# Optimization experiments

Measured on AMD Instinct MI355X. Metric: run time of the kernel, lower is better.

The kernel has to match this reference:

```python
import jax, jax.numpy as jnp
import numpy as np

N_COMP = 36          # sdf_n_comp
GRID = 300           # gridSize per axis
SDF_DIM = 256
APP_DIM = 128
MULTIRES = 3         # sdf positional-encoding octaves -> 3 + 3*2*3 = 21 channels
N_PTS = 524288       # sample points per batch (~1024 rays x 512 samples)
EMB_CH = 3 + 3 * 2 * MULTIRES            # 21
IN_CH = EMB_CH + 3 * N_COMP              # 129
OUT_CH = 1 + APP_DIM                     # 129 (sdf + appearance feature)
INIT_RADIUS = 0.2


def setup_inputs() -> dict:
    key = jax.random.key(0)
    ks = jax.random.split(key, 6)
    xyz_sampled = jax.random.uniform(ks[0], (N_PTS, 3), jnp.float32) * 2.0 - 1.0
    # tensor-decomposition grids (stacked over the 3 VM planes)
    planes = jax.random.normal(ks[1], (3, N_COMP, GRID, GRID), jnp.float32) * 0.1
    lines = jax.random.normal(ks[2], (3, N_COMP, GRID), jnp.float32) * (1.0 / (N_COMP * 3))
    # sdf_mat MLP params, initialized per init_mlp()
    w1 = jax.random.normal(ks[3], (SDF_DIM, IN_CH), jnp.float32) * (np.sqrt(2.0) / np.sqrt(SDF_DIM))
    b1 = jnp.zeros((SDF_DIM,), jnp.float32)
    w2 = jax.random.normal(ks[4], (OUT_CH, SDF_DIM), jnp.float32) * 1e-4 + np.sqrt(np.pi) / np.sqrt(SDF_DIM)
    b2 = jnp.full((OUT_CH,), -INIT_RADIUS, jnp.float32)
    return {"xyz_sampled": xyz_sampled, "planes": planes, "lines": lines,
            "w1": w1, "b1": b1, "w2": w2, "b2": b2}


def _bilin2d(plane, x, y):
    """Bilinear grid_sample, align_corners=True. plane [C,H,W]; x,y [N] in [-1,1] -> [C,N]."""
    C, H, W = plane.shape
    fx = (x + 1.0) * 0.5 * (W - 1)
    fy = (y + 1.0) * 0.5 * (H - 1)
    x0 = jnp.clip(jnp.floor(fx).astype(jnp.int32), 0, W - 2)
    y0 = jnp.clip(jnp.floor(fy).astype(jnp.int32), 0, H - 2)
    tx = fx - x0
    ty = fy - y0
    v00 = plane[:, y0, x0]
    v01 = plane[:, y0, x0 + 1]
    v10 = plane[:, y0 + 1, x0]
    v11 = plane[:, y0 + 1, x0 + 1]
    return (v00 * (1 - tx) * (1 - ty) + v01 * tx * (1 - ty)
            + v10 * (1 - tx) * ty + v11 * tx * ty)


def _lin1d(line, z):
    """Linear grid_sample, align_corners=True. line [C,L]; z [N] in [-1,1] -> [C,N]."""
    C, L = line.shape
    fz = (z + 1.0) * 0.5 * (L - 1)
    z0 = jnp.clip(jnp.floor(fz).astype(jnp.int32), 0, L - 2)
    tz = fz - z0
    return line[:, z0] * (1 - tz) + line[:, z0 + 1] * tz


def _embed(x):
    """NeRF positional encoding, include_input, octaves 2^0..2^(MULTIRES-1). [N,3] -> [N,21]."""
    freqs = 2.0 ** jnp.arange(MULTIRES, dtype=x.dtype)
    ang = x[:, :, None] * freqs  # [N,3,MULTIRES]
    n = x.shape[0]
    return jnp.concatenate([x, jnp.sin(ang).reshape(n, -1), jnp.cos(ang).reshape(n, -1)], axis=-1)


def reference(xyz_sampled, planes, lines, w1, b1, w2, b2):
    # aabb = [-1,1]^3 -> normalization is identity, kept explicit for faithfulness
    xn = (xyz_sampled - (-1.0)) / 2.0 * 2.0 - 1.0
    # matMode=[[0,1],[0,2],[1,2]], vecMode=[2,1,0]
    px = jnp.stack([xn[:, 0], xn[:, 0], xn[:, 1]])  # [3,N] first plane coord
    py = jnp.stack([xn[:, 1], xn[:, 2], xn[:, 2]])  # [3,N] second plane coord
    pz = jnp.stack([xn[:, 2], xn[:, 1], xn[:, 0]])  # [3,N] line coord
    pf = jax.vmap(_bilin2d)(planes, px, py)         # [3,C,N]
    lf = jax.vmap(_lin1d)(lines, pz)                # [3,C,N]
    feat = (pf * lf).transpose(2, 0, 1).reshape(xn.shape[0], -1)  # [N, 3*C]
    mlp_in = jnp.concatenate([_embed(xyz_sampled), feat], axis=-1)  # [N, 129]
    h = jax.nn.softplus(100.0 * (mlp_in @ w1.T + b1)) / 100.0       # Softplus(beta=100)
    out = h @ w2.T + b2                                             # [N, 1+app_dim]
    return out
```

## Files before the change

kernel.cpp:

```cpp
#include <hip/hip_runtime.h>
#include <hip/hip_bf16.h>
#include <cstdint>
#include <cstddef>


using half2v = __attribute__((ext_vector_type(2))) _Float16;
using half4  = __attribute__((ext_vector_type(4))) _Float16;
using half8  = __attribute__((ext_vector_type(8))) _Float16;
using floatx4 = __attribute__((ext_vector_type(4))) float;

#define NPTS    524288
#define GRES    300
#define NCOMP   36
#define SDFD    256
#define IN_CH   129
#define IN_PAD  160
#define OUT_CH  129
#define OUT_PAD 144
#define TILE_M  64
#define S_IN    168
#define S_H     264

#define OFF_W1S 0
#define SZ_W1S  (5*4*256*8*2)
#define OFF_W2S (OFF_W1S + SZ_W1S)
#define SZ_W2S  (8*4*144*8*2)
#define OFF_PLT (OFF_W2S + SZ_W2S)
#define SZ_PLT  (3*300*300*36*2)
#define OFF_LT  (OFF_PLT + SZ_PLT)
#define SZ_LT   (3*300*36*2)
#define WS_NEED_FAST ((size_t)(OFF_LT + SZ_LT))


__global__ void prep_planes_k(const float* __restrict__ planes, _Float16* __restrict__ pl_t) {
    int idx = blockIdx.x * 256 + threadIdx.x;
    if (idx >= 3 * GRES * GRES) return;
    int x = idx % GRES; int t = idx / GRES; int y = t % GRES; int m = t / GRES;
    _Float16* dst = pl_t + (size_t)idx * NCOMP;
    const float* src = planes + (size_t)m * NCOMP * GRES * GRES + (size_t)y * GRES + x;
    #pragma unroll
    for (int c4 = 0; c4 < NCOMP; c4 += 4) {
        half4 o;
        #pragma unroll
        for (int i = 0; i < 4; ++i)
            o[i] = (_Float16)src[(size_t)(c4 + i) * GRES * GRES];
        *(half4*)(dst + c4) = o;
    }
}

#define NB_W1 ((5*4*256*8 + 255)/256)
#define NB_W2 ((8*4*144*8 + 255)/256)
#define NB_L  ((3*GRES + 255)/256)
__global__ void prep_small_k(const float* __restrict__ w1, const float* __restrict__ w2,
                             const float* __restrict__ lines,
                             _Float16* __restrict__ w1s, _Float16* __restrict__ w2s,
                             _Float16* __restrict__ l_t) {
    int b = blockIdx.x;
    if (b < NB_W1) {
        int t = b * 256 + threadIdx.x;
        if (t >= 5 * 4 * 256 * 8) return;
        int j = t & 7; int n = (t >> 3) & 255; int q = t >> 11;
        int k = (q >> 2) * 32 + (q & 3) * 8 + j;
        float v = 0.f;
        if (k < IN_CH) {
            int ko = (k < 108) ? (21 + k) : (k - 108);
            v = w1[n * IN_CH + ko];
        }
        w1s[t] = (_Float16)v;
    } else if (b < NB_W1 + NB_W2) {
        int t = (b - NB_W1) * 256 + threadIdx.x;
        if (t >= 8 * 4 * 144 * 8) return;
        int j = t & 7; int r = t >> 3; int n = r % 144; int q = r / 144;
        int k = (q >> 2) * 32 + (q & 3) * 8 + j;
        float v = (n < OUT_CH) ? w2[n * SDFD + k] : 0.f;
        w2s[t] = (_Float16)v;
    } else {
        int idx = (b - NB_W1 - NB_W2) * 256 + threadIdx.x;
        if (idx >= 3 * GRES) return;
        int z = idx % GRES; int m = idx / GRES;
        _Float16* dst = l_t + (size_t)idx * NCOMP;
        const float* src = lines + ((size_t)m * NCOMP) * GRES + z;
        for (int c = 0; c < NCOMP; ++c)
            dst[c] = (_Float16)src[(size_t)c * GRES];
    }
}


__device__ __forceinline__ float softplus100(float z) {
    return fmaxf(z, 0.f) + __logf(1.f + __expf(-fabsf(z)));
}

template <bool FAST>
__global__ __launch_bounds__(256, 2)
void tsdf_fused_k(const float* __restrict__ xyz,
                  const float* __restrict__ planes,
                  const float* __restrict__ lines,
                  const _Float16* __restrict__ pl_t,
                  const _Float16* __restrict__ l_t,
                  const _Float16* __restrict__ w1s,
                  const _Float16* __restrict__ w2s,
                  const float* __restrict__ b1,
                  const float* __restrict__ b2,
                  float* __restrict__ out)
{
    __shared__ _Float16 mlp_lds[TILE_M * S_IN];
    __shared__ _Float16 h_lds[TILE_M * S_H];
    const int tid = threadIdx.x;
    const int blk = blockIdx.x;

    {
        const int p   = tid >> 2;
        const int sub = tid & 3;
        const size_t gp = (size_t)blk * TILE_M + p;
        const float X = xyz[gp * 3 + 0];
        const float Y = xyz[gp * 3 + 1];
        const float Z = xyz[gp * 3 + 2];
        if (sub < 3) {
            const int m = sub;
            const float px = (m == 2) ? Y : X;
            const float py = (m == 0) ? Y : Z;
            const float pz = (m == 0) ? Z : ((m == 1) ? Y : X);
            float fx = (px + 1.f) * 0.5f * 299.f;
            float fy = (py + 1.f) * 0.5f * 299.f;
            float fz = (pz + 1.f) * 0.5f * 299.f;
            int x0 = (int)floorf(fx); x0 = x0 < 0 ? 0 : (x0 > 298 ? 298 : x0);
            int y0 = (int)floorf(fy); y0 = y0 < 0 ? 0 : (y0 > 298 ? 298 : y0);
            int z0 = (int)floorf(fz); z0 = z0 < 0 ? 0 : (z0 > 298 ? 298 : z0);
            const float tx = fx - (float)x0, ty = fy - (float)y0, tz = fz - (float)z0;
            const float w00 = (1.f - tx) * (1.f - ty), w01 = tx * (1.f - ty);
            const float w10 = (1.f - tx) * ty,         w11 = tx * ty;
            const float lw0 = 1.f - tz, lw1 = tz;
            _Float16* dst = &mlp_lds[p * S_IN + m * NCOMP];
            if (FAST) {
                const _Float16 h00 = (_Float16)w00, h01 = (_Float16)w01;
                const _Float16 h10 = (_Float16)w10, h11 = (_Float16)w11;
                const _Float16 hl0 = (_Float16)lw0, hl1 = (_Float16)lw1;
                const half4 W00 = {h00, h00, h00, h00}, W01 = {h01, h01, h01, h01};
                const half4 W10 = {h10, h10, h10, h10}, W11 = {h11, h11, h11, h11};
                const half4 WL0 = {hl0, hl0, hl0, hl0}, WL1 = {hl1, hl1, hl1, hl1};
                const _Float16* b00 = pl_t + ((size_t)(m * GRES + y0) * GRES + x0) * NCOMP;
                const _Float16* lb  = l_t + (size_t)(m * GRES + z0) * NCOMP;
                #pragma unroll
                for (int c = 0; c < NCOMP; c += 4) {
                    half4 v00 = *(const half4*)(b00 + c);
                    half4 v01 = *(const half4*)(b00 + NCOMP + c);
                    half4 v10 = *(const half4*)(b00 + GRES * NCOMP + c);
                    half4 v11 = *(const half4*)(b00 + GRES * NCOMP + NCOMP + c);
                    half4 l0  = *(const half4*)(lb + c);
                    half4 l1  = *(const half4*)(lb + NCOMP + c);
                    half4 pf = v00 * W00 + v01 * W01 + v10 * W10 + v11 * W11;
                    half4 lf = l0 * WL0 + l1 * WL1;
                    *(half4*)(dst + c) = pf * lf;
                }
            } else {
                const float* pb = planes + (size_t)m * NCOMP * GRES * GRES;
                for (int c = 0; c < NCOMP; ++c) {
                    const float* pc = pb + (size_t)c * GRES * GRES + (size_t)y0 * GRES + x0;
                    const float* lc = lines + ((size_t)m * NCOMP + c) * GRES + z0;
                    float pf = pc[0] * w00 + pc[1] * w01 + pc[GRES] * w10 + pc[GRES + 1] * w11;
                    float lf = lc[0] * lw0 + lc[1] * lw1;
                    dst[c] = (_Float16)(pf * lf);
                }
            }
        } else {
            _Float16* e = &mlp_lds[p * S_IN];
            e[108] = (_Float16)X; e[109] = (_Float16)Y; e[110] = (_Float16)Z;
            const float v3[3] = {X, Y, Z};
            #pragma unroll
            for (int d = 0; d < 3; ++d) {
                float f = 1.f;
                #pragma unroll
                for (int q = 0; q < 3; ++q) {
                    const float a = v3[d] * f;
                    e[111 + d * 3 + q] = (_Float16)__sinf(a);
                    e[120 + d * 3 + q] = (_Float16)__cosf(a);
                    f *= 2.f;
                }
            }
            e[129] = (_Float16)0.f;
            #pragma unroll
            for (int k = 130; k < IN_PAD; k += 2)
                *(half2v*)&e[k] = (half2v){(_Float16)0.f, (_Float16)0.f};
        }
    }
    __syncthreads();

    const int lane = tid & 63;
    const int wv   = tid >> 6;
    const int l15  = lane & 15;
    const int quad = lane >> 4;

    floatx4 acc1[4][4];
    #pragma unroll
    for (int mt = 0; mt < 4; ++mt)
        #pragma unroll
        for (int nt = 0; nt < 4; ++nt)
            acc1[mt][nt] = (floatx4){0.f, 0.f, 0.f, 0.f};

    #pragma unroll
    for (int s = 0; s < 5; ++s) {
        half8 a[4], b[4];
        #pragma unroll
        for (int mt = 0; mt < 4; ++mt)
            a[mt] = *(const half8*)&mlp_lds[(mt * 16 + l15) * S_IN + s * 32 + quad * 8];
        #pragma unroll
        for (int nt = 0; nt < 4; ++nt)
            b[nt] = *(const half8*)&w1s[((size_t)(s * 4 + quad) * 256 + wv * 64 + nt * 16 + l15) * 8];
        #pragma unroll
        for (int mt = 0; mt < 4; ++mt)
            #pragma unroll
            for (int nt = 0; nt < 4; ++nt)
                acc1[mt][nt] = __builtin_amdgcn_mfma_f32_16x16x32_f16(a[mt], b[nt], acc1[mt][nt], 0, 0, 0);
    }
    #pragma unroll
    for (int nt = 0; nt < 4; ++nt) {
        const int n = wv * 64 + nt * 16 + l15;
        const float bias = b1[n];
        #pragma unroll
        for (int mt = 0; mt < 4; ++mt) {
            #pragma unroll
            for (int r = 0; r < 4; ++r) {
                const float z = 100.f * (acc1[mt][nt][r] + bias);
                h_lds[(mt * 16 + quad * 4 + r) * S_H + n] = (_Float16)(softplus100(z) * 0.01f);
            }
        }
    }
    __syncthreads();

    floatx4 acc2[9];
    #pragma unroll
    for (int nt = 0; nt < 9; ++nt) acc2[nt] = (floatx4){0.f, 0.f, 0.f, 0.f};

    #pragma unroll
    for (int s = 0; s < 8; ++s) {
        const half8 a = *(const half8*)&h_lds[(wv * 16 + l15) * S_H + s * 32 + quad * 8];
        #pragma unroll
        for (int nt = 0; nt < 9; ++nt) {
            const half8 b = *(const half8*)&w2s[((size_t)(s * 4 + quad) * 144 + nt * 16 + l15) * 8];
            acc2[nt] = __builtin_amdgcn_mfma_f32_16x16x32_f16(a, b, acc2[nt], 0, 0, 0);
        }
    }
    const int m_lo = wv * 16 + quad * 4;
    #pragma unroll
    for (int nt = 0; nt < 9; ++nt) {
        const int n = nt * 16 + l15;
        if (n < OUT_CH) {
            const float bias = b2[n];
            #pragma unroll
            for (int r = 0; r < 4; ++r) {
                const size_t gm = (size_t)blk * TILE_M + m_lo + r;
                out[gm * OUT_CH + n] = acc2[nt][r] + bias;
            }
        }
    }
}


extern "C" void kernel_launch(void* const* d_in, const int* in_sizes, int n_in,
                              void* d_out, int out_size, void* d_ws, size_t ws_size,
                              hipStream_t stream) {
    const float* xyz    = (const float*)d_in[0];
    const float* planes = (const float*)d_in[1];
    const float* lines  = (const float*)d_in[2];
    const float* w1     = (const float*)d_in[3];
    const float* b1     = (const float*)d_in[4];
    const float* w2     = (const float*)d_in[5];
    const float* b2     = (const float*)d_in[6];
    float* out = (float*)d_out;
    char* ws = (char*)d_ws;

    _Float16* w1s  = (_Float16*)(ws + OFF_W1S);
    _Float16* w2s  = (_Float16*)(ws + OFF_W2S);
    _Float16* pl_t = (_Float16*)(ws + OFF_PLT);
    _Float16* l_t  = (_Float16*)(ws + OFF_LT);

    const bool fast = (ws_size >= WS_NEED_FAST);

    prep_small_k<<<NB_W1 + NB_W2 + NB_L, 256, 0, stream>>>(w1, w2, lines, w1s, w2s, l_t);

    if (fast) {
        prep_planes_k<<<(3 * GRES * GRES + 255) / 256, 256, 0, stream>>>(planes, pl_t);
        tsdf_fused_k<true><<<NPTS / TILE_M, 256, 0, stream>>>(
            xyz, planes, lines, pl_t, l_t, w1s, w2s, b1, b2, out);
    } else {
        tsdf_fused_k<false><<<NPTS / TILE_M, 256, 0, stream>>>(
            xyz, planes, lines, pl_t, l_t, w1s, w2s, b1, b2, out);
    }
}
```

Baseline: 579.1 us.

## Pad channels to 40, split sampling and MLP into two kernels, swizzle LDS

Pads the plane and line channel layouts from 36 to 40 so gathers can use half8 vector loads, and reorders the W1 K-layout to match. When the workspace is large enough, the fused kernel is split in two. A sampler kernel writes MFMA-ready A-fragments to a global staging buffer, and a separate MLP kernel reads them directly. LDS row padding is replaced with XOR swizzles. The split is meant to raise occupancy and decouple latency-bound gathers from MFMA work, at the cost of a 160 MB intermediate round trip through memory.

```diff
diff --git a/kernel.cpp b/kernel.cpp
--- a/kernel.cpp
+++ b/kernel.cpp
@@ -1,50 +1,51 @@
 #include <hip/hip_runtime.h>
-#include <hip/hip_bf16.h>
 #include <cstdint>
 #include <cstddef>
 
 
-using half2v = __attribute__((ext_vector_type(2))) _Float16;
-using half4  = __attribute__((ext_vector_type(4))) _Float16;
-using half8  = __attribute__((ext_vector_type(8))) _Float16;
+using half2v  = __attribute__((ext_vector_type(2))) _Float16;
+using half4   = __attribute__((ext_vector_type(4))) _Float16;
+using half8   = __attribute__((ext_vector_type(8))) _Float16;
 using floatx4 = __attribute__((ext_vector_type(4))) float;
 
 #define NPTS    524288
 #define GRES    300
 #define NCOMP   36
+#define NCP     40
 #define SDFD    256
 #define IN_CH   129
-#define IN_PAD  160
 #define OUT_CH  129
-#define OUT_PAD 144
 #define TILE_M  64
-#define S_IN    168
-#define S_H     264
 
 #define OFF_W1S 0
 #define SZ_W1S  (5*4*256*8*2)
 #define OFF_W2S (OFF_W1S + SZ_W1S)
 #define SZ_W2S  (8*4*144*8*2)
-#define OFF_PLT (OFF_W2S + SZ_W2S)
-#define SZ_PLT  (3*300*300*36*2)
-#define OFF_LT  (OFF_PLT + SZ_PLT)
-#define SZ_LT   (3*300*36*2)
-#define WS_NEED_FAST ((size_t)(OFF_LT + SZ_LT))
+#define OFF_LT  (OFF_W2S + SZ_W2S)
+#define SZ_LT   (3*GRES*NCP*2)
+#define OFF_PLT (OFF_LT + SZ_LT)
+#define SZ_PLT  ((size_t)3*GRES*GRES*NCP*2)
+#define OFF_MLP (OFF_PLT + SZ_PLT)
+#define SZ_MLP  ((size_t)NPTS*160*2)
+#define NEED_T1 ((size_t)OFF_PLT + SZ_PLT)
+#define NEED_T0 ((size_t)OFF_MLP + SZ_MLP)
 
 
 __global__ void prep_planes_k(const float* __restrict__ planes, _Float16* __restrict__ pl_t) {
     int idx = blockIdx.x * 256 + threadIdx.x;
     if (idx >= 3 * GRES * GRES) return;
     int x = idx % GRES; int t = idx / GRES; int y = t % GRES; int m = t / GRES;
-    _Float16* dst = pl_t + (size_t)idx * NCOMP;
+    _Float16* dst = pl_t + (size_t)idx * NCP;
     const float* src = planes + (size_t)m * NCOMP * GRES * GRES + (size_t)y * GRES + x;
     #pragma unroll
-    for (int c4 = 0; c4 < NCOMP; c4 += 4) {
-        half4 o;
-        #pragma unroll
-        for (int i = 0; i < 4; ++i)
-            o[i] = (_Float16)src[(size_t)(c4 + i) * GRES * GRES];
-        *(half4*)(dst + c4) = o;
+    for (int j = 0; j < 5; ++j) {
+        half8 o;
+        #pragma unroll
+        for (int e = 0; e < 8; ++e) {
+            int c = j * 8 + e;
+            o[e] = (c < NCOMP) ? (_Float16)src[(size_t)c * GRES * GRES] : (_Float16)0.f;
+        }
+        *(half8*)(dst + j * 8) = o;
     }
 }
 
@@ -58,30 +59,32 @@
     int b = blockIdx.x;
     if (b < NB_W1) {
         int t = b * 256 + threadIdx.x;
-        if (t >= 5 * 4 * 256 * 8) return;
         int j = t & 7; int n = (t >> 3) & 255; int q = t >> 11;
-        int k = (q >> 2) * 32 + (q & 3) * 8 + j;
+        int k = q * 8 + j;
         float v = 0.f;
-        if (k < IN_CH) {
-            int ko = (k < 108) ? (21 + k) : (k - 108);
-            v = w1[n * IN_CH + ko];
+        if (k < 120) {
+            int m = k / 40, c = k % 40;
+            if (c < NCOMP) v = w1[n * IN_CH + 21 + m * NCOMP + c];
+        } else if (k < 141) {
+            v = w1[n * IN_CH + (k - 120)];
         }
         w1s[t] = (_Float16)v;
     } else if (b < NB_W1 + NB_W2) {
         int t = (b - NB_W1) * 256 + threadIdx.x;
-        if (t >= 8 * 4 * 144 * 8) return;
+        if (t >= 8*4*144*8) return;
         int j = t & 7; int r = t >> 3; int n = r % 144; int q = r / 144;
-        int k = (q >> 2) * 32 + (q & 3) * 8 + j;
+        int k = q * 8 + j;
         float v = (n < OUT_CH) ? w2[n * SDFD + k] : 0.f;
         w2s[t] = (_Float16)v;
     } else {
         int idx = (b - NB_W1 - NB_W2) * 256 + threadIdx.x;
         if (idx >= 3 * GRES) return;
         int z = idx % GRES; int m = idx / GRES;
-        _Float16* dst = l_t + (size_t)idx * NCOMP;
+        _Float16* dst = l_t + (size_t)idx * NCP;
         const float* src = lines + ((size_t)m * NCOMP) * GRES + z;
-        for (int c = 0; c < NCOMP; ++c)
-            dst[c] = (_Float16)src[(size_t)c * GRES];
+        #pragma unroll
+        for (int c = 0; c < NCOMP; ++c) dst[c] = (_Float16)src[(size_t)c * GRES];
+        dst[36] = dst[37] = dst[38] = dst[39] = (_Float16)0.f;
     }
 }
 
@@ -90,106 +93,253 @@
     return fmaxf(z, 0.f) + __logf(1.f + __expf(-fabsf(z)));
 }
 
-template <bool FAST>
-__global__ __launch_bounds__(256, 2)
-void tsdf_fused_k(const float* __restrict__ xyz,
-                  const float* __restrict__ planes,
-                  const float* __restrict__ lines,
-                  const _Float16* __restrict__ pl_t,
-                  const _Float16* __restrict__ l_t,
-                  const _Float16* __restrict__ w1s,
-                  const _Float16* __restrict__ w2s,
-                  const float* __restrict__ b1,
-                  const float* __restrict__ b2,
-                  float* __restrict__ out)
+__device__ __forceinline__ void plane_coords(int m, float X, float Y, float Z,
+                                             int& x0, int& y0, int& z0,
+                                             float& tx, float& ty, float& tz) {
+    const float px = (m == 2) ? Y : X;
+    const float py = (m == 0) ? Y : Z;
+    const float pz = (m == 0) ? Z : ((m == 1) ? Y : X);
+    float fx = (px + 1.f) * 0.5f * 299.f;
+    float fy = (py + 1.f) * 0.5f * 299.f;
+    float fz = (pz + 1.f) * 0.5f * 299.f;
+    x0 = (int)floorf(fx); x0 = x0 < 0 ? 0 : (x0 > 298 ? 298 : x0);
+    y0 = (int)floorf(fy); y0 = y0 < 0 ? 0 : (y0 > 298 ? 298 : y0);
+    z0 = (int)floorf(fz); z0 = z0 < 0 ? 0 : (z0 > 298 ? 298 : z0);
+    tx = fx - (float)x0; ty = fy - (float)y0; tz = fz - (float)z0;
+}
+
+__device__ __forceinline__ void plane_gather_fast(
+    int m, float X, float Y, float Z,
+    const _Float16* __restrict__ pl_t, const _Float16* __restrict__ l_t,
+    half8 f[5])
 {
-    __shared__ _Float16 mlp_lds[TILE_M * S_IN];
-    __shared__ _Float16 h_lds[TILE_M * S_H];
+    int x0, y0, z0; float tx, ty, tz;
+    plane_coords(m, X, Y, Z, x0, y0, z0, tx, ty, tz);
+    const _Float16 h00 = (_Float16)((1.f - tx) * (1.f - ty));
+    const _Float16 h01 = (_Float16)(tx * (1.f - ty));
+    const _Float16 h10 = (_Float16)((1.f - tx) * ty);
+    const _Float16 h11 = (_Float16)(tx * ty);
+    const _Float16 hl0 = (_Float16)(1.f - tz), hl1 = (_Float16)tz;
+    const half8 W00 = {h00,h00,h00,h00,h00,h00,h00,h00};
+    const half8 W01 = {h01,h01,h01,h01,h01,h01,h01,h01};
+    const half8 W10 = {h10,h10,h10,h10,h10,h10,h10,h10};
+    const half8 W11 = {h11,h11,h11,h11,h11,h11,h11,h11};
+    const half8 WL0 = {hl0,hl0,hl0,hl0,hl0,hl0,hl0,hl0};
+    const half8 WL1 = {hl1,hl1,hl1,hl1,hl1,hl1,hl1,hl1};
+    const _Float16* r0 = pl_t + ((size_t)(m * GRES + y0) * GRES + x0) * NCP;
+    const _Float16* r1 = r0 + (size_t)GRES * NCP;
+    const _Float16* lb = l_t + (size_t)(m * GRES + z0) * NCP;
+    half8 a0[10], a1[10], al[10];
+    #pragma unroll
+    for (int j = 0; j < 10; ++j) a0[j] = *(const half8*)(r0 + 8 * j);
+    #pragma unroll
+    for (int j = 0; j < 10; ++j) a1[j] = *(const half8*)(r1 + 8 * j);
+    half8 pf[5];
+    #pragma unroll
+    for (int j = 0; j < 5; ++j)
+        pf[j] = a0[j] * W00 + a0[j + 5] * W01 + a1[j] * W10 + a1[j + 5] * W11;
+    #pragma unroll
+    for (int j = 0; j < 10; ++j) al[j] = *(const half8*)(lb + 8 * j);
+    #pragma unroll
+    for (int j = 0; j < 5; ++j) {
+        half8 lf = al[j] * WL0 + al[j + 5] * WL1;
+        f[j] = pf[j] * lf;
+    }
+}
+
+__device__ __forceinline__ void plane_gather_slow(
+    int m, float X, float Y, float Z,
+    const float* __restrict__ planes, const float* __restrict__ lines,
+    half8 f[5])
+{
+    int x0, y0, z0; float tx, ty, tz;
+    plane_coords(m, X, Y, Z, x0, y0, z0, tx, ty, tz);
+    const float w00 = (1.f - tx) * (1.f - ty), w01 = tx * (1.f - ty);
+    const float w10 = (1.f - tx) * ty,         w11 = tx * ty;
+    const float lw0 = 1.f - tz, lw1 = tz;
+    #pragma unroll
+    for (int j = 0; j < 5; ++j) f[j] = (half8){0,0,0,0,0,0,0,0};
+    const float* pb = planes + (size_t)m * NCOMP * GRES * GRES;
+    #pragma unroll
+    for (int c = 0; c < NCOMP; ++c) {
+        const float* pc = pb + (size_t)c * GRES * GRES + (size_t)y0 * GRES + x0;
+        const float* lc = lines + ((size_t)m * NCOMP + c) * GRES + z0;
+        float pf = pc[0] * w00 + pc[1] * w01 + pc[GRES] * w10 + pc[GRES + 1] * w11;
+        float lf = lc[0] * lw0 + lc[1] * lw1;
+        f[c >> 3][c & 7] = (_Float16)(pf * lf);
+    }
+}
+
+__device__ __forceinline__ void embed_chunks(float X, float Y, float Z, half8 e[5]) {
+    const float v3[3] = {X, Y, Z};
+    _Float16 s[3][3], c[3][3];
+    #pragma unroll
+    for (int d = 0; d < 3; ++d) {
+        float fm = 1.f;
+        #pragma unroll
+        for (int q = 0; q < 3; ++q) {
+            const float a = v3[d] * fm;
+            s[d][q] = (_Float16)__sinf(a);
+            c[d][q] = (_Float16)__cosf(a);
+            fm *= 2.f;
+        }
+    }
+    const _Float16 z0 = (_Float16)0.f;
+    e[0] = (half8){(_Float16)X, (_Float16)Y, (_Float16)Z, s[0][0], s[0][1], s[0][2], s[1][0], s[1][1]};
+    e[1] = (half8){s[1][2], s[2][0], s[2][1], s[2][2], c[0][0], c[0][1], c[0][2], c[1][0]};
+    e[2] = (half8){c[1][1], c[1][2], c[2][0], c[2][1], c[2][2], z0, z0, z0};
+    e[3] = (half8){z0,z0,z0,z0,z0,z0,z0,z0};
+    e[4] = (half8){z0,z0,z0,z0,z0,z0,z0,z0};
+}
+
+
+__global__ __launch_bounds__(256, 4)
+void sampler_k(const float* __restrict__ xyz,
+               const _Float16* __restrict__ pl_t,
+               const _Float16* __restrict__ l_t,
+               _Float16* __restrict__ mg)
+{
     const int tid = threadIdx.x;
-    const int blk = blockIdx.x;
+    const size_t gp = (size_t)blockIdx.x * TILE_M + (tid >> 2);
+    const int sub = tid & 3;
+    const float X = xyz[gp * 3 + 0];
+    const float Y = xyz[gp * 3 + 1];
+    const float Z = xyz[gp * 3 + 2];
+    const size_t tile = gp >> 6;
+    const int row = (int)(gp & 63);
+    _Float16* base = mg + ((size_t)tile * 1280 + row) * 8;
+    half8 f[5];
+    if (sub < 3) {
+        plane_gather_fast(sub, X, Y, Z, pl_t, l_t, f);
+        #pragma unroll
+        for (int j = 0; j < 5; ++j)
+            *(half8*)(base + (size_t)(sub * 5 + j) * 512) = f[j];
+    } else {
+        embed_chunks(X, Y, Z, f);
+        #pragma unroll
+        for (int j = 0; j < 5; ++j)
+            *(half8*)(base + (size_t)(15 + j) * 512) = f[j];
+    }
+}
+
+
+__global__ __launch_bounds__(256, 4)
+void mlp_k(const _Float16* __restrict__ mg,
+           const _Float16* __restrict__ w1s, const _Float16* __restrict__ w2s,
+           const float* __restrict__ b1, const float* __restrict__ b2,
+           float* __restrict__ out)
+{
+    __shared__ _Float16 h_lds[TILE_M * 256];
+    const int tid = threadIdx.x, blk = blockIdx.x;
+    const int lane = tid & 63, wv = tid >> 6, l15 = lane & 15, quad = lane >> 4;
+    const _Float16* tg = mg + (size_t)blk * (1280 * 8);
+
+    floatx4 acc1[4][4];
+    #pragma unroll
+    for (int mt = 0; mt < 4; ++mt)
+        #pragma unroll
+        for (int nt = 0; nt < 4; ++nt)
+            acc1[mt][nt] = (floatx4){0.f, 0.f, 0.f, 0.f};
+
+    #pragma unroll
+    for (int s = 0; s < 5; ++s) {
+        half8 a[4], b[4];
+        #pragma unroll
+        for (int mt = 0; mt < 4; ++mt)
+            a[mt] = *(const half8*)(tg + ((size_t)((s * 4 + quad) * 64) + mt * 16 + l15) * 8);
+        #pragma unroll
+        for (int nt = 0; nt < 4; ++nt)
+            b[nt] = *(const half8*)(w1s + ((size_t)((s * 4 + quad) * 256) + wv * 64 + nt * 16 + l15) * 8);
+        #pragma unroll
+        for (int mt = 0; mt < 4; ++mt)
+            #pragma unroll
+            for (int nt = 0; nt < 4; ++nt)
+                acc1[mt][nt] = __builtin_amdgcn_mfma_f32_16x16x32_f16(a[mt], b[nt], acc1[mt][nt], 0, 0, 0);
+    }
+    #pragma unroll
+    for (int nt = 0; nt < 4; ++nt) {
+        const int n = wv * 64 + nt * 16 + l15;
+        const float bias = b1[n];
+        #pragma unroll
+        for (int mt = 0; mt < 4; ++mt) {
+            #pragma unroll
+            for (int r = 0; r < 4; ++r) {
+                const int rowh = mt * 16 + quad * 4 + r;
+                const float z = 100.f * (acc1[mt][nt][r] + bias);
+                h_lds[(rowh * 256 + n) ^ ((rowh & 7) << 3)] = (_Float16)(softplus100(z) * 0.01f);
+            }
+        }
+    }
+    __syncthreads();
+
+    floatx4 acc2[9];
+    #pragma unroll
+    for (int nt = 0; nt < 9; ++nt) acc2[nt] = (floatx4){0.f, 0.f, 0.f, 0.f};
+
+    const int row2 = wv * 16 + l15;
+    #pragma unroll
+    for (int s = 0; s < 8; ++s) {
+        const half8 a = *(const half8*)&h_lds[(row2 * 256 + s * 32 + quad * 8) ^ ((row2 & 7) << 3)];
+        #pragma unroll
+        for (int nt = 0; nt < 9; ++nt) {
+            const half8 b = *(const half8*)(w2s + ((size_t)((s * 4 + quad) * 144) + nt * 16 + l15) * 8);
+            acc2[nt] = __builtin_amdgcn_mfma_f32_16x16x32_f16(a, b, acc2[nt], 0, 0, 0);
+        }
+    }
+    const int m_lo = wv * 16 + quad * 4;
+    #pragma unroll
+    for (int nt = 0; nt < 9; ++nt) {
+        const int n = nt * 16 + l15;
+        if (n < OUT_CH) {
+            const float bias = b2[n];
+            #pragma unroll
+            for (int r = 0; r < 4; ++r) {
+                const size_t gm = (size_t)blk * TILE_M + m_lo + r;
+                out[gm * OUT_CH + n] = acc2[nt][r] + bias;
+            }
+        }
+    }
+}
+
+
+template <int FASTMODE>
+__global__ __launch_bounds__(256, 3)
+void tsdf_fused40_k(const float* __restrict__ xyz,
+                    const float* __restrict__ planes, const float* __restrict__ lines,
+                    const _Float16* __restrict__ pl_t, const _Float16* __restrict__ l_t,
+                    const _Float16* __restrict__ w1s, const _Float16* __restrict__ w2s,
+                    const float* __restrict__ b1, const float* __restrict__ b2,
+                    float* __restrict__ out)
+{
+    __shared__ _Float16 mlp_lds[TILE_M * 160];
+    __shared__ _Float16 h_lds[TILE_M * 256];
+    const int tid = threadIdx.x, blk = blockIdx.x;
 
     {
-        const int p   = tid >> 2;
-        const int sub = tid & 3;
+        const int p = tid >> 2, sub = tid & 3;
         const size_t gp = (size_t)blk * TILE_M + p;
         const float X = xyz[gp * 3 + 0];
         const float Y = xyz[gp * 3 + 1];
         const float Z = xyz[gp * 3 + 2];
+        half8 f[5];
+        int c0;
         if (sub < 3) {
-            const int m = sub;
-            const float px = (m == 2) ? Y : X;
-            const float py = (m == 0) ? Y : Z;
-            const float pz = (m == 0) ? Z : ((m == 1) ? Y : X);
-            float fx = (px + 1.f) * 0.5f * 299.f;
-            float fy = (py + 1.f) * 0.5f * 299.f;
-            float fz = (pz + 1.f) * 0.5f * 299.f;
-            int x0 = (int)floorf(fx); x0 = x0 < 0 ? 0 : (x0 > 298 ? 298 : x0);
-            int y0 = (int)floorf(fy); y0 = y0 < 0 ? 0 : (y0 > 298 ? 298 : y0);
-            int z0 = (int)floorf(fz); z0 = z0 < 0 ? 0 : (z0 > 298 ? 298 : z0);
-            const float tx = fx - (float)x0, ty = fy - (float)y0, tz = fz - (float)z0;
-            const float w00 = (1.f - tx) * (1.f - ty), w01 = tx * (1.f - ty);
-            const float w10 = (1.f - tx) * ty,         w11 = tx * ty;
-            const float lw0 = 1.f - tz, lw1 = tz;
-            _Float16* dst = &mlp_lds[p * S_IN + m * NCOMP];
-            if (FAST) {
-                const _Float16 h00 = (_Float16)w00, h01 = (_Float16)w01;
-                const _Float16 h10 = (_Float16)w10, h11 = (_Float16)w11;
-                const _Float16 hl0 = (_Float16)lw0, hl1 = (_Float16)lw1;
-                const half4 W00 = {h00, h00, h00, h00}, W01 = {h01, h01, h01, h01};
-                const half4 W10 = {h10, h10, h10, h10}, W11 = {h11, h11, h11, h11};
-                const half4 WL0 = {hl0, hl0, hl0, hl0}, WL1 = {hl1, hl1, hl1, hl1};
-                const _Float16* b00 = pl_t + ((size_t)(m * GRES + y0) * GRES + x0) * NCOMP;
-                const _Float16* lb  = l_t + (size_t)(m * GRES + z0) * NCOMP;
-                #pragma unroll
-                for (int c = 0; c < NCOMP; c += 4) {
-                    half4 v00 = *(const half4*)(b00 + c);
-                    half4 v01 = *(const half4*)(b00 + NCOMP + c);
-                    half4 v10 = *(const half4*)(b00 + GRES * NCOMP + c);
-                    half4 v11 = *(const half4*)(b00 + GRES * NCOMP + NCOMP + c);
-                    half4 l0  = *(const half4*)(lb + c);
-                    half4 l1  = *(const half4*)(lb + NCOMP + c);
-                    half4 pf = v00 * W00 + v01 * W01 + v10 * W10 + v11 * W11;
-                    half4 lf = l0 * WL0 + l1 * WL1;
-                    *(half4*)(dst + c) = pf * lf;
-                }
-            } else {
-                const float* pb = planes + (size_t)m * NCOMP * GRES * GRES;
-                for (int c = 0; c < NCOMP; ++c) {
-                    const float* pc = pb + (size_t)c * GRES * GRES + (size_t)y0 * GRES + x0;
-                    const float* lc = lines + ((size_t)m * NCOMP + c) * GRES + z0;
-                    float pf = pc[0] * w00 + pc[1] * w01 + pc[GRES] * w10 + pc[GRES + 1] * w11;
-                    float lf = lc[0] * lw0 + lc[1] * lw1;
-                    dst[c] = (_Float16)(pf * lf);
-                }
-            }
+            if (FASTMODE) plane_gather_fast(sub, X, Y, Z, pl_t, l_t, f);
+            else          plane_gather_slow(sub, X, Y, Z, planes, lines, f);
+            c0 = sub * 5;
         } else {
-            _Float16* e = &mlp_lds[p * S_IN];
-            e[108] = (_Float16)X; e[109] = (_Float16)Y; e[110] = (_Float16)Z;
-            const float v3[3] = {X, Y, Z};
-            #pragma unroll
-            for (int d = 0; d < 3; ++d) {
-                float f = 1.f;
-                #pragma unroll
-                for (int q = 0; q < 3; ++q) {
-                    const float a = v3[d] * f;
-                    e[111 + d * 3 + q] = (_Float16)__sinf(a);
-                    e[120 + d * 3 + q] = (_Float16)__cosf(a);
-                    f *= 2.f;
-                }
-            }
-            e[129] = (_Float16)0.f;
-            #pragma unroll
-            for (int k = 130; k < IN_PAD; k += 2)
-                *(half2v*)&e[k] = (half2v){(_Float16)0.f, (_Float16)0.f};
+            embed_chunks(X, Y, Z, f);
+            c0 = 15;
+        }
+        #pragma unroll
+        for (int j = 0; j < 5; ++j) {
+            const int idx = (p * 160 + (c0 + j) * 8) ^ ((p & 3) << 3);
+            *(half8*)&mlp_lds[idx] = f[j];
         }
     }
     __syncthreads();
 
-    const int lane = tid & 63;
-    const int wv   = tid >> 6;
-    const int l15  = lane & 15;
-    const int quad = lane >> 4;
-
+    const int lane = tid & 63, wv = tid >> 6, l15 = lane & 15, quad = lane >> 4;
     floatx4 acc1[4][4];
     #pragma unroll
     for (int mt = 0; mt < 4; ++mt)
@@ -201,11 +351,13 @@
     for (int s = 0; s < 5; ++s) {
         half8 a[4], b[4];
         #pragma unroll
-        for (int mt = 0; mt < 4; ++mt)
-            a[mt] = *(const half8*)&mlp_lds[(mt * 16 + l15) * S_IN + s * 32 + quad * 8];
+        for (int mt = 0; mt < 4; ++mt) {
+            const int row = mt * 16 + l15;
+            a[mt] = *(const half8*)&mlp_lds[(row * 160 + s * 32 + quad * 8) ^ ((row & 3) << 3)];
+        }
         #pragma unroll
         for (int nt = 0; nt < 4; ++nt)
-            b[nt] = *(const half8*)&w1s[((size_t)(s * 4 + quad) * 256 + wv * 64 + nt * 16 + l15) * 8];
+            b[nt] = *(const half8*)(w1s + ((size_t)((s * 4 + quad) * 256) + wv * 64 + nt * 16 + l15) * 8);
         #pragma unroll
         for (int mt = 0; mt < 4; ++mt)
             #pragma unroll
@@ -220,8 +372,9 @@
         for (int mt = 0; mt < 4; ++mt) {
             #pragma unroll
             for (int r = 0; r < 4; ++r) {
+                const int rowh = mt * 16 + quad * 4 + r;
                 const float z = 100.f * (acc1[mt][nt][r] + bias);
-                h_lds[(mt * 16 + quad * 4 + r) * S_H + n] = (_Float16)(softplus100(z) * 0.01f);
+                h_lds[(rowh * 256 + n) ^ ((rowh & 7) << 3)] = (_Float16)(softplus100(z) * 0.01f);
             }
         }
     }
@@ -231,12 +384,13 @@
     #pragma unroll
     for (int nt = 0; nt < 9; ++nt) acc2[nt] = (floatx4){0.f, 0.f, 0.f, 0.f};
 
+    const int row2 = wv * 16 + l15;
     #pragma unroll
     for (int s = 0; s < 8; ++s) {
-        const half8 a = *(const half8*)&h_lds[(wv * 16 + l15) * S_H + s * 32 + quad * 8];
+        const half8 a = *(const half8*)&h_lds[(row2 * 256 + s * 32 + quad * 8) ^ ((row2 & 7) << 3)];
         #pragma unroll
         for (int nt = 0; nt < 9; ++nt) {
-            const half8 b = *(const half8*)&w2s[((size_t)(s * 4 + quad) * 144 + nt * 16 + l15) * 8];
+            const half8 b = *(const half8*)(w2s + ((size_t)((s * 4 + quad) * 144) + nt * 16 + l15) * 8);
             acc2[nt] = __builtin_amdgcn_mfma_f32_16x16x32_f16(a, b, acc2[nt], 0, 0, 0);
         }
     }
@@ -271,19 +425,25 @@
 
     _Float16* w1s  = (_Float16*)(ws + OFF_W1S);
     _Float16* w2s  = (_Float16*)(ws + OFF_W2S);
+    _Float16* l_t  = (_Float16*)(ws + OFF_LT);
     _Float16* pl_t = (_Float16*)(ws + OFF_PLT);
-    _Float16* l_t  = (_Float16*)(ws + OFF_LT);
-
-    const bool fast = (ws_size >= WS_NEED_FAST);
+    _Float16* mg   = (_Float16*)(ws + OFF_MLP);
+
+    const bool t0 = (ws_size >= NEED_T0);
+    const bool t1 = (ws_size >= NEED_T1);
 
     prep_small_k<<<NB_W1 + NB_W2 + NB_L, 256, 0, stream>>>(w1, w2, lines, w1s, w2s, l_t);
 
-    if (fast) {
+    if (t0) {
         prep_planes_k<<<(3 * GRES * GRES + 255) / 256, 256, 0, stream>>>(planes, pl_t);
-        tsdf_fused_k<true><<<NPTS / TILE_M, 256, 0, stream>>>(
+        sampler_k<<<NPTS / TILE_M, 256, 0, stream>>>(xyz, pl_t, l_t, mg);
+        mlp_k<<<NPTS / TILE_M, 256, 0, stream>>>(mg, w1s, w2s, b1, b2, out);
+    } else if (t1) {
+        prep_planes_k<<<(3 * GRES * GRES + 255) / 256, 256, 0, stream>>>(planes, pl_t);
+        tsdf_fused40_k<1><<<NPTS / TILE_M, 256, 0, stream>>>(
             xyz, planes, lines, pl_t, l_t, w1s, w2s, b1, b2, out);
     } else {
-        tsdf_fused_k<false><<<NPTS / TILE_M, 256, 0, stream>>>(
+        tsdf_fused40_k<0><<<NPTS / TILE_M, 256, 0, stream>>>(
             xyz, planes, lines, pl_t, l_t, w1s, w2s, b1, b2, out);
     }
 }
```

New measurement: 680.7 us. 17.5% more time.
